# Optimization experiments

Hardware: AMD Instinct MI355X
Metric: run time of the kernel (lower is better)

Reference implementation:

```python
import jax, jax.numpy as jnp
import numpy as np

B, N, DIN, DOUT, H = 4, 2048, 512, 512, 8
HD = DOUT // H


def setup_inputs() -> dict:
    key = jax.random.key(0)
    ks = jax.random.split(key, 8)
    x = jax.random.normal(ks[0], (B, N, DIN), dtype=jnp.float32)
    mask = jax.random.randint(ks[1], (B, 1, N, N), 0, 2, dtype=jnp.int32)
    s = 1.0 / np.sqrt(DIN)
    Wq = jax.random.uniform(ks[2], (DOUT, DIN), jnp.float32, -s, s)
    Wk = jax.random.uniform(ks[3], (DOUT, DIN), jnp.float32, -s, s)
    Wv = jax.random.uniform(ks[4], (DOUT, DIN), jnp.float32, -s, s)
    bq = jax.random.uniform(ks[5], (DOUT,), jnp.float32, -s, s)
    bk = jax.random.uniform(ks[6], (DOUT,), jnp.float32, -s, s)
    bv = jax.random.uniform(ks[7], (DOUT,), jnp.float32, -s, s)
    return {"x": x, "Wq": Wq, "bq": bq, "Wk": Wk, "bk": bk, "Wv": Wv, "bv": bv, "mask": mask}


def reference(x, Wq, bq, Wk, bk, Wv, bv, mask):
    b, n, _ = x.shape
    # torch Linear: y = x @ W.T + b ; split heads -> [b, h, n, hd]
    def proj(W, bias):
        y = jnp.einsum('bnd,od->bno', x, W) + bias
        return y.reshape(b, n, H, HD).transpose(0, 2, 1, 3)
    Q, K, V = proj(Wq, bq), proj(Wk, bk), proj(Wv, bv)
    scores = jnp.einsum('bhnd,bhmd->bhnm', Q, K) / np.sqrt(HD).astype(np.float32)
    scores = jnp.where(mask == 0, jnp.float32(-1e9), scores)
    attn = jax.nn.softmax(scores, axis=-1)
    ctx = jnp.einsum('bhnm,bhmd->bhnd', attn, V)
    ctx = ctx.transpose(0, 2, 1, 3).reshape(b, n, DOUT)
    return jax.nn.elu(ctx)
```

## Files before the change

### kernel.cpp

```cpp
#include <hip/hip_runtime.h>
#include <math.h>
#include <stdint.h>

#define CB 4
#define CN 2048
#define CDIN 512
#define CDOUT 512
#define CH 8
#define CHD 64
#define CM (CB * CN)
#define CBH (CB * CH)
#define NKT (CN / 64)

typedef _Float16 f16x8 __attribute__((ext_vector_type(8)));
typedef _Float16 f16x4 __attribute__((ext_vector_type(4)));
typedef float    f32x4 __attribute__((ext_vector_type(4)));

#define QSCALE 0.1803368801111204f

#define PB_X  2048
#define PB_WQ 2176
#define PB_WK 2304
#define PB_WV 2432
#define PB_MB 3456

__global__ __launch_bounds__(256) void prep_kernel(
    const float* __restrict__ x,  _Float16* __restrict__ xh,
    const float* __restrict__ Wq, _Float16* __restrict__ wqh,
    const float* __restrict__ Wk, _Float16* __restrict__ wkh,
    const float* __restrict__ Wv, _Float16* __restrict__ wvh,
    const int* __restrict__ mask, unsigned long long* __restrict__ mbits)
{
    const int bx = blockIdx.x;
    if (bx >= PB_WV) {
        const int lane = threadIdx.x & 63;
        const int wv   = threadIdx.x >> 6;
        const int wbase = (bx - PB_WV) * 256 + wv * 64;
        unsigned long long myword = 0;
        #pragma unroll 8
        for (int it = 0; it < 64; ++it) {
            int v = mask[(size_t)(wbase + it) * 64 + lane];
            unsigned long long bal = __ballot(v != 0);
            if (lane == it) myword = bal;
        }
        mbits[wbase + lane] = myword;
        return;
    }
    const float* s; _Float16* d; int i;
    if (bx < PB_X)       { s = x;  d = xh;  i = bx * 2048 + threadIdx.x * 8; }
    else if (bx < PB_WQ) { s = Wq; d = wqh; i = (bx - PB_X)  * 2048 + threadIdx.x * 8; }
    else if (bx < PB_WK) { s = Wk; d = wkh; i = (bx - PB_WQ) * 2048 + threadIdx.x * 8; }
    else                 { s = Wv; d = wvh; i = (bx - PB_WK) * 2048 + threadIdx.x * 8; }
    float4 a = *(const float4*)&s[i];
    float4 b = *(const float4*)&s[i + 4];
    f16x8 h = {(_Float16)a.x, (_Float16)a.y, (_Float16)a.z, (_Float16)a.w,
               (_Float16)b.x, (_Float16)b.y, (_Float16)b.z, (_Float16)b.w};
    *(f16x8*)&d[i] = h;
}

__global__ __launch_bounds__(256) void proj_kernel(
    const _Float16* __restrict__ xh,
    const _Float16* __restrict__ Wqh, const float* __restrict__ bq,
    const _Float16* __restrict__ Wkh, const float* __restrict__ bk,
    const _Float16* __restrict__ Wvh, const float* __restrict__ bv,
    _Float16* __restrict__ Qf, _Float16* __restrict__ Kf, _Float16* __restrict__ Vt)
{
    const int z = blockIdx.z;
    const _Float16* W; const float* bias;
    if (z == 0)      { W = Wqh; bias = bq; }
    else if (z == 1) { W = Wkh; bias = bk; }
    else             { W = Wvh; bias = bv; }

    __shared__ _Float16 SM[2 * 128 * 72];

    const int tid  = threadIdx.x;
    const int m0   = blockIdx.x * 128;
    const int o0   = blockIdx.y * 128;
    const int lane = tid & 63, w = tid >> 6;
    const int il   = lane & 15, quad = lane >> 4;
    const int srow = tid >> 3, kc = (tid & 7) * 8;

    f32x4 acc[2][8] = {};
    f16x8 xr[4], wr[4];

    #pragma unroll
    for (int i = 0; i < 4; ++i) {
        xr[i] = *(const f16x8*)&xh[(size_t)(m0 + srow + i * 32) * CDIN + kc];
        wr[i] = *(const f16x8*)&W[(size_t)(o0 + srow + i * 32) * CDIN + kc];
    }

    for (int k0 = 0; k0 < CDIN; k0 += 64) {
        #pragma unroll
        for (int i = 0; i < 4; ++i) {
            *(f16x8*)&SM[(srow + i * 32) * 72 + kc] = xr[i];
            *(f16x8*)&SM[9216 + (srow + i * 32) * 72 + kc] = wr[i];
        }
        __syncthreads();

        if (k0 + 64 < CDIN) {
            #pragma unroll
            for (int i = 0; i < 4; ++i) {
                xr[i] = *(const f16x8*)&xh[(size_t)(m0 + srow + i * 32) * CDIN + k0 + 64 + kc];
                wr[i] = *(const f16x8*)&W[(size_t)(o0 + srow + i * 32) * CDIN + k0 + 64 + kc];
            }
        }

        #pragma unroll
        for (int dh = 0; dh < 2; ++dh) {
            f16x8 X0 = *(const f16x8*)&SM[(w * 32 + il) * 72 + dh * 32 + quad * 8];
            f16x8 X1 = *(const f16x8*)&SM[(w * 32 + 16 + il) * 72 + dh * 32 + quad * 8];
            if (z < 2) {
                #pragma unroll
                for (int s = 0; s < 8; ++s) {
                    f16x8 Wv_ = *(const f16x8*)&SM[9216 + (s * 16 + il) * 72 + dh * 32 + quad * 8];
                    acc[0][s] = __builtin_amdgcn_mfma_f32_16x16x32_f16(Wv_, X0, acc[0][s], 0, 0, 0);
                    acc[1][s] = __builtin_amdgcn_mfma_f32_16x16x32_f16(Wv_, X1, acc[1][s], 0, 0, 0);
                }
            } else {
                #pragma unroll
                for (int s = 0; s < 8; ++s) {
                    f16x8 Wv_ = *(const f16x8*)&SM[9216 + (s * 16 + il) * 72 + dh * 32 + quad * 8];
                    acc[0][s] = __builtin_amdgcn_mfma_f32_16x16x32_f16(X0, Wv_, acc[0][s], 0, 0, 0);
                    acc[1][s] = __builtin_amdgcn_mfma_f32_16x16x32_f16(X1, Wv_, acc[1][s], 0, 0, 0);
                }
            }
        }
        __syncthreads();
    }

    const int b  = m0 / CN;
    const int nb = m0 & (CN - 1);
    if (z < 2) {
        const float sc = (z == 0) ? QSCALE : 1.0f;
        #pragma unroll
        for (int s = 0; s < 8; ++s) {
            #pragma unroll
            for (int mi = 0; mi < 2; ++mi) {
                f16x4 pv;
                #pragma unroll
                for (int r = 0; r < 4; ++r)
                    pv[r] = (_Float16)((acc[mi][s][r] + bias[o0 + s * 16 + quad * 4 + r]) * sc);
                *(f16x4*)&SM[(w * 32 + mi * 16 + il) * 140 + s * 16 + quad * 4] = pv;
            }
        }
    } else {
        #pragma unroll
        for (int s = 0; s < 8; ++s) {
            const float bval = bias[o0 + s * 16 + il];
            #pragma unroll
            for (int mi = 0; mi < 2; ++mi) {
                f16x4 pv = {(_Float16)(acc[mi][s][0] + bval),
                            (_Float16)(acc[mi][s][1] + bval),
                            (_Float16)(acc[mi][s][2] + bval),
                            (_Float16)(acc[mi][s][3] + bval)};
                *(f16x4*)&SM[(s * 16 + il) * 140 + w * 32 + mi * 16 + quad * 4] = pv;
            }
        }
    }
    __syncthreads();

    const int uu   = tid & 127;
    const int hseg = tid >> 7;
    const int bh   = b * CH + (o0 >> 6) + hseg;
    if (z < 2) {
        _Float16* dst = ((z == 0) ? Qf : Kf) + ((size_t)bh * CN + nb) * CHD;
        #pragma unroll
        for (int k = 0; k < 8; ++k) {
            int n = k * 16 + (uu >> 3);
            int d = (uu & 7) * 8;
            *(f16x8*)&dst[(size_t)n * CHD + d] =
                *(const f16x8*)&SM[n * 140 + hseg * 64 + d];
        }
    } else {
        _Float16* dst = Vt + (size_t)bh * CHD * CN + nb;
        #pragma unroll
        for (int k = 0; k < 8; ++k) {
            int d = k * 8 + (uu >> 4);
            int n = (uu & 15) * 8;
            *(f16x8*)&dst[(size_t)d * CN + n] =
                *(const f16x8*)&SM[(hseg * 64 + d) * 140 + n];
        }
    }
}

__global__ __launch_bounds__(512, 4) void attn_kernel(
    const _Float16* __restrict__ Qf, const _Float16* __restrict__ Kf,
    const _Float16* __restrict__ Vt, const unsigned long long* __restrict__ mbits,
    float* __restrict__ out)
{
    __shared__ uint4 Ks4[2][64][8];
    __shared__ uint4 Vs4[2][64][8];
    __shared__ uint4 Ps4[8][32][8];

    const int tid  = threadIdx.x;
    const int q0   = blockIdx.x * 128;
    const int bh   = blockIdx.y;
    const int b    = bh >> 3, h = bh & 7;
    const int lane = tid & 63, w = tid >> 6;
    const int kg   = w >> 2;
    const int wi   = w & 3;
    const int il   = lane & 15, quad = lane >> 4;
    const int i7   = il & 7;

    const int gtid = tid & 255;
    const int srow = gtid >> 2;
    const int sg   = (gtid & 3) * 2;
    const int sw0  = sg       ^ (srow & 7);
    const int sw1  = (sg + 1) ^ (srow & 7);

    const int kb = kg * 1024;

    _Float16* Pw = (_Float16*)&Ps4[w][0][0];

    const _Float16* Qb = Qf + (size_t)bh * CN * CHD;
    const _Float16* Kb = Kf + (size_t)bh * CN * CHD;
    const _Float16* Vb = Vt + (size_t)bh * CHD * CN;

    const int qg0 = q0 + wi * 32 + il;
    const int qg1 = qg0 + 16;
    const unsigned long long* mrow0 = mbits + ((size_t)b * CN + qg0) * NKT + kg * 16;
    const unsigned long long* mrow1 = mbits + ((size_t)b * CN + qg1) * NKT + kg * 16;

    f16x8 Qa[2][2];
    Qa[0][0] = *(const f16x8*)&Qb[(size_t)qg0 * CHD + quad * 8];
    Qa[0][1] = *(const f16x8*)&Qb[(size_t)qg0 * CHD + 32 + quad * 8];
    Qa[1][0] = *(const f16x8*)&Qb[(size_t)qg1 * CHD + quad * 8];
    Qa[1][1] = *(const f16x8*)&Qb[(size_t)qg1 * CHD + 32 + quad * 8];

    const f16x8 ones = {1.f16, 1.f16, 1.f16, 1.f16, 1.f16, 1.f16, 1.f16, 1.f16};

    f32x4 oacc[2][4] = {};
    f32x4 lacc[2] = {};

    uint4 kA0, kA1, vA0, vA1;
    unsigned long long mn0, mn1;
    kA0 = *(const uint4*)&Kb[(size_t)(kb + srow) * CHD + sg * 8];
    kA1 = *(const uint4*)&Kb[(size_t)(kb + srow) * CHD + sg * 8 + 8];
    vA0 = *(const uint4*)&Vb[(size_t)srow * CN + kb + sg * 8];
    vA1 = *(const uint4*)&Vb[(size_t)srow * CN + kb + sg * 8 + 8];
    mn0 = mrow0[0];
    mn1 = mrow1[0];
    Ks4[kg][srow][sw0] = kA0; Ks4[kg][srow][sw1] = kA1;
    Vs4[kg][srow][sw0] = vA0; Vs4[kg][srow][sw1] = vA1;
    __syncthreads();

    for (int t = 0; t < 16; ++t) {
        const unsigned long long mc0 = mn0, mc1 = mn1;

        if (t < 15) {
            const size_t ko = (size_t)(kb + (t + 1) * 64 + srow) * CHD + sg * 8;
            kA0 = *(const uint4*)&Kb[ko];
            kA1 = *(const uint4*)&Kb[ko + 8];
            const size_t vo = (size_t)srow * CN + kb + (t + 1) * 64 + sg * 8;
            vA0 = *(const uint4*)&Vb[vo];
            vA1 = *(const uint4*)&Vb[vo + 8];
            mn0 = mrow0[t + 1];
            mn1 = mrow1[t + 1];
        }

        f32x4 st[2][4] = {};
        #pragma unroll
        for (int s = 0; s < 4; ++s) {
            f16x8 A0 = *(const f16x8*)&Ks4[kg][s * 16 + il][quad ^ i7];
            f16x8 A1 = *(const f16x8*)&Ks4[kg][s * 16 + il][(4 + quad) ^ i7];
            st[0][s] = __builtin_amdgcn_mfma_f32_16x16x32_f16(A0, Qa[0][0], st[0][s], 0, 0, 0);
            st[0][s] = __builtin_amdgcn_mfma_f32_16x16x32_f16(A1, Qa[0][1], st[0][s], 0, 0, 0);
            st[1][s] = __builtin_amdgcn_mfma_f32_16x16x32_f16(A0, Qa[1][0], st[1][s], 0, 0, 0);
            st[1][s] = __builtin_amdgcn_mfma_f32_16x16x32_f16(A1, Qa[1][1], st[1][s], 0, 0, 0);
        }

        #pragma unroll
        for (int g = 0; g < 2; ++g) {
            const unsigned long long mw = g ? mc1 : mc0;
            const uint32_t mlo = (uint32_t)mw, mhi = (uint32_t)(mw >> 32);
            #pragma unroll
            for (int s = 0; s < 4; ++s) {
                const uint32_t mm = (s < 2) ? mlo : mhi;
                const int base = ((s & 1) << 4) + quad * 4;
                f16x4 pv;
                #pragma unroll
                for (int r = 0; r < 4; ++r) {
                    float sv = ((mm >> (base + r)) & 1u) ? st[g][s][r] : -1e9f;
                    pv[r] = (_Float16)__builtin_amdgcn_exp2f(sv);
                }
                const int pg = (s * 2 + (quad >> 1)) ^ i7;
                *(f16x4*)&Pw[(g * 16 + il) * 64 + pg * 8 + (quad & 1) * 4] = pv;
            }
        }

        f16x8 Pa[2][2];
        #pragma unroll
        for (int g = 0; g < 2; ++g) {
            Pa[g][0] = *(const f16x8*)&Pw[(g * 16 + il) * 64 + (quad ^ i7) * 8];
            Pa[g][1] = *(const f16x8*)&Pw[(g * 16 + il) * 64 + ((4 + quad) ^ i7) * 8];
        }
        #pragma unroll
        for (int s = 0; s < 4; ++s) {
            f16x8 B0 = *(const f16x8*)&Vs4[kg][s * 16 + il][quad ^ i7];
            f16x8 B1 = *(const f16x8*)&Vs4[kg][s * 16 + il][(4 + quad) ^ i7];
            oacc[0][s] = __builtin_amdgcn_mfma_f32_16x16x32_f16(Pa[0][0], B0, oacc[0][s], 0, 0, 0);
            oacc[0][s] = __builtin_amdgcn_mfma_f32_16x16x32_f16(Pa[0][1], B1, oacc[0][s], 0, 0, 0);
            oacc[1][s] = __builtin_amdgcn_mfma_f32_16x16x32_f16(Pa[1][0], B0, oacc[1][s], 0, 0, 0);
            oacc[1][s] = __builtin_amdgcn_mfma_f32_16x16x32_f16(Pa[1][1], B1, oacc[1][s], 0, 0, 0);
        }
        lacc[0] = __builtin_amdgcn_mfma_f32_16x16x32_f16(Pa[0][0], ones, lacc[0], 0, 0, 0);
        lacc[0] = __builtin_amdgcn_mfma_f32_16x16x32_f16(Pa[0][1], ones, lacc[0], 0, 0, 0);
        lacc[1] = __builtin_amdgcn_mfma_f32_16x16x32_f16(Pa[1][0], ones, lacc[1], 0, 0, 0);
        lacc[1] = __builtin_amdgcn_mfma_f32_16x16x32_f16(Pa[1][1], ones, lacc[1], 0, 0, 0);

        if (t < 15) {
            __syncthreads();
            Ks4[kg][srow][sw0] = kA0; Ks4[kg][srow][sw1] = kA1;
            Vs4[kg][srow][sw0] = vA0; Vs4[kg][srow][sw1] = vA1;
            __syncthreads();
        }
    }

    __syncthreads();
    f32x4* Ob = (f32x4*)&Ps4[0][0][0];
    f32x4* Lb = (f32x4*)&Ks4[0][0][0];
    const int obase = (wi * 64 + lane) * 8;
    const int lbase = (wi * 64 + lane) * 2;
    if (kg == 1) {
        #pragma unroll
        for (int g = 0; g < 2; ++g)
            #pragma unroll
            for (int s = 0; s < 4; ++s)
                Ob[obase + ((g * 4 + s) ^ (lane & 7))] = oacc[g][s];
        Lb[lbase + (lane & 1)]       = lacc[0];
        Lb[lbase + ((lane & 1) ^ 1)] = lacc[1];
    }
    __syncthreads();
    if (kg == 0) {
        lacc[0] += Lb[lbase + (lane & 1)];
        lacc[1] += Lb[lbase + ((lane & 1) ^ 1)];
        #pragma unroll
        for (int g = 0; g < 2; ++g)
            #pragma unroll
            for (int s = 0; s < 4; ++s)
                oacc[g][s] += Ob[obase + ((g * 4 + s) ^ (lane & 7))];

        #pragma unroll
        for (int g = 0; g < 2; ++g) {
            #pragma unroll
            for (int s = 0; s < 4; ++s) {
                const int d = h * CHD + s * 16 + il;
                #pragma unroll
                for (int r = 0; r < 4; ++r) {
                    int n = q0 + wi * 32 + g * 16 + quad * 4 + r;
                    float c = oacc[g][s][r] / lacc[g][r];
                    out[((size_t)b * CN + n) * CDOUT + d] = c > 0.f ? c : expm1f(c);
                }
            }
        }
    }
}

extern "C" void kernel_launch(void* const* d_in, const int* in_sizes, int n_in,
                              void* d_out, int out_size, void* d_ws, size_t ws_size,
                              hipStream_t stream) {
    const float* x    = (const float*)d_in[0];
    const float* Wq   = (const float*)d_in[1];
    const float* bq   = (const float*)d_in[2];
    const float* Wk   = (const float*)d_in[3];
    const float* bk   = (const float*)d_in[4];
    const float* Wv   = (const float*)d_in[5];
    const float* bv   = (const float*)d_in[6];
    const int*   mask = (const int*)d_in[7];
    float* out = (float*)d_out;

    const size_t nx = (size_t)CM * CDIN;
    const size_t nw = (size_t)CDOUT * CDIN;
    const size_t nt = (size_t)CBH * CN * CHD;
    _Float16* xh  = (_Float16*)d_ws;
    _Float16* wqh = xh + nx;
    _Float16* wkh = wqh + nw;
    _Float16* wvh = wkh + nw;
    _Float16* Qf  = wvh + nw;
    _Float16* Kf  = Qf + nt;
    _Float16* Vt  = Kf + nt;
    unsigned long long* mbits = (unsigned long long*)(Vt + nt);

    prep_kernel<<<dim3(PB_MB), 256, 0, stream>>>(
        x, xh, Wq, wqh, Wk, wkh, Wv, wvh, mask, mbits);
    proj_kernel<<<dim3(CM / 128, CDOUT / 128, 3), 256, 0, stream>>>(
        xh, wqh, bq, wkh, bk, wvh, bv, Qf, Kf, Vt);
    attn_kernel<<<dim3(CN / 128, CBH), 512, 0, stream>>>(
        Qf, Kf, Vt, mbits, out);
}
```

Baseline: 216.0 us.

## Use direct global-to-LDS loads in projection, swizzle attention grid, add MFMA priorities

Rewrites the projection GEMM to load tiles straight from global memory into XOR-swizzled, double-buffered LDS with global_load_lds, replacing the register-staged copy and one barrier per k-step. It also splits the prep kernel into separate convert and mask-packing launches and runs the projection as three launches, one per matrix. In attention it remaps blocks so consecutive blocks spread across heads and query tiles, and raises wave priority around the MFMA sections. The extra launches add overhead, and the block remap changes L2 locality.

Result: slower. 333.5 us (+54.4%).

```diff
diff --git a/kernel.cpp b/kernel.cpp
--- a/kernel.cpp
+++ b/kernel.cpp
@@ -18,34 +18,24 @@
 
 #define QSCALE 0.1803368801111204f
 
+__device__ __forceinline__ void gl_lds16(const _Float16* g, _Float16* l) {
+    __builtin_amdgcn_global_load_lds(
+        (const __attribute__((address_space(1))) void*)g,
+        (__attribute__((address_space(3))) void*)l, 16, 0, 0);
+}
+
 #define PB_X  2048
 #define PB_WQ 2176
 #define PB_WK 2304
 #define PB_WV 2432
-#define PB_MB 3456
-
-__global__ __launch_bounds__(256) void prep_kernel(
+
+__global__ __launch_bounds__(256) void prep_cvt_kernel(
     const float* __restrict__ x,  _Float16* __restrict__ xh,
     const float* __restrict__ Wq, _Float16* __restrict__ wqh,
     const float* __restrict__ Wk, _Float16* __restrict__ wkh,
-    const float* __restrict__ Wv, _Float16* __restrict__ wvh,
-    const int* __restrict__ mask, unsigned long long* __restrict__ mbits)
+    const float* __restrict__ Wv, _Float16* __restrict__ wvh)
 {
     const int bx = blockIdx.x;
-    if (bx >= PB_WV) {
-        const int lane = threadIdx.x & 63;
-        const int wv   = threadIdx.x >> 6;
-        const int wbase = (bx - PB_WV) * 256 + wv * 64;
-        unsigned long long myword = 0;
-        #pragma unroll 8
-        for (int it = 0; it < 64; ++it) {
-            int v = mask[(size_t)(wbase + it) * 64 + lane];
-            unsigned long long bal = __ballot(v != 0);
-            if (lane == it) myword = bal;
-        }
-        mbits[wbase + lane] = myword;
-        return;
-    }
     const float* s; _Float16* d; int i;
     if (bx < PB_X)       { s = x;  d = xh;  i = bx * 2048 + threadIdx.x * 8; }
     else if (bx < PB_WQ) { s = Wq; d = wqh; i = (bx - PB_X)  * 2048 + threadIdx.x * 8; }
@@ -58,68 +48,85 @@
     *(f16x8*)&d[i] = h;
 }
 
+__global__ __launch_bounds__(256) void prep_mask_kernel(
+    const int* __restrict__ mask, unsigned long long* __restrict__ mbits)
+{
+    const int lane = threadIdx.x & 63;
+    const int wv   = threadIdx.x >> 6;
+    const int wbase = blockIdx.x * 256 + wv * 64;
+    unsigned long long myword = 0;
+    #pragma unroll 8
+    for (int it = 0; it < 64; ++it) {
+        int v = mask[(size_t)(wbase + it) * 64 + lane];
+        unsigned long long bal = __ballot(v != 0);
+        if (lane == it) myword = bal;
+    }
+    mbits[wbase + lane] = myword;
+}
+
 __global__ __launch_bounds__(256) void proj_kernel(
     const _Float16* __restrict__ xh,
     const _Float16* __restrict__ Wqh, const float* __restrict__ bq,
     const _Float16* __restrict__ Wkh, const float* __restrict__ bk,
     const _Float16* __restrict__ Wvh, const float* __restrict__ bv,
-    _Float16* __restrict__ Qf, _Float16* __restrict__ Kf, _Float16* __restrict__ Vt)
+    _Float16* __restrict__ Qf, _Float16* __restrict__ Kf, _Float16* __restrict__ Vt,
+    const int z)
 {
-    const int z = blockIdx.z;
     const _Float16* W; const float* bias;
     if (z == 0)      { W = Wqh; bias = bq; }
     else if (z == 1) { W = Wkh; bias = bk; }
     else             { W = Wvh; bias = bv; }
 
-    __shared__ _Float16 SM[2 * 128 * 72];
+    __shared__ _Float16 SH[2][2][128][64];
 
     const int tid  = threadIdx.x;
     const int m0   = blockIdx.x * 128;
     const int o0   = blockIdx.y * 128;
     const int lane = tid & 63, w = tid >> 6;
     const int il   = lane & 15, quad = lane >> 4;
-    const int srow = tid >> 3, kc = (tid & 7) * 8;
+    const int i7   = il & 7;
+
+    const int srow8 = lane >> 3;
+    const int srcg  = ((lane & 7) ^ srow8) * 8;
 
     f32x4 acc[2][8] = {};
-    f16x8 xr[4], wr[4];
 
     #pragma unroll
     for (int i = 0; i < 4; ++i) {
-        xr[i] = *(const f16x8*)&xh[(size_t)(m0 + srow + i * 32) * CDIN + kc];
-        wr[i] = *(const f16x8*)&W[(size_t)(o0 + srow + i * 32) * CDIN + kc];
-    }
-
-    for (int k0 = 0; k0 < CDIN; k0 += 64) {
-        #pragma unroll
-        for (int i = 0; i < 4; ++i) {
-            *(f16x8*)&SM[(srow + i * 32) * 72 + kc] = xr[i];
-            *(f16x8*)&SM[9216 + (srow + i * 32) * 72 + kc] = wr[i];
-        }
-        __syncthreads();
-
+        const int r0 = i * 32 + w * 8;
+        gl_lds16(&xh[(size_t)(m0 + r0 + srow8) * CDIN + srcg], &SH[0][0][r0][0]);
+        gl_lds16(&W [(size_t)(o0 + r0 + srow8) * CDIN + srcg], &SH[1][0][r0][0]);
+    }
+    __syncthreads();
+
+    int kb = 0;
+    for (int k0 = 0; k0 < CDIN; k0 += 64, kb ^= 1) {
         if (k0 + 64 < CDIN) {
             #pragma unroll
             for (int i = 0; i < 4; ++i) {
-                xr[i] = *(const f16x8*)&xh[(size_t)(m0 + srow + i * 32) * CDIN + k0 + 64 + kc];
-                wr[i] = *(const f16x8*)&W[(size_t)(o0 + srow + i * 32) * CDIN + k0 + 64 + kc];
+                const int r0 = i * 32 + w * 8;
+                gl_lds16(&xh[(size_t)(m0 + r0 + srow8) * CDIN + k0 + 64 + srcg],
+                         &SH[0][kb ^ 1][r0][0]);
+                gl_lds16(&W [(size_t)(o0 + r0 + srow8) * CDIN + k0 + 64 + srcg],
+                         &SH[1][kb ^ 1][r0][0]);
             }
         }
 
         #pragma unroll
         for (int dh = 0; dh < 2; ++dh) {
-            f16x8 X0 = *(const f16x8*)&SM[(w * 32 + il) * 72 + dh * 32 + quad * 8];
-            f16x8 X1 = *(const f16x8*)&SM[(w * 32 + 16 + il) * 72 + dh * 32 + quad * 8];
+            f16x8 X0 = *(const f16x8*)&SH[0][kb][w * 32 + il][((dh * 4 + quad) ^ i7) * 8];
+            f16x8 X1 = *(const f16x8*)&SH[0][kb][w * 32 + 16 + il][((dh * 4 + quad) ^ i7) * 8];
             if (z < 2) {
                 #pragma unroll
                 for (int s = 0; s < 8; ++s) {
-                    f16x8 Wv_ = *(const f16x8*)&SM[9216 + (s * 16 + il) * 72 + dh * 32 + quad * 8];
+                    f16x8 Wv_ = *(const f16x8*)&SH[1][kb][s * 16 + il][((dh * 4 + quad) ^ i7) * 8];
                     acc[0][s] = __builtin_amdgcn_mfma_f32_16x16x32_f16(Wv_, X0, acc[0][s], 0, 0, 0);
                     acc[1][s] = __builtin_amdgcn_mfma_f32_16x16x32_f16(Wv_, X1, acc[1][s], 0, 0, 0);
                 }
             } else {
                 #pragma unroll
                 for (int s = 0; s < 8; ++s) {
-                    f16x8 Wv_ = *(const f16x8*)&SM[9216 + (s * 16 + il) * 72 + dh * 32 + quad * 8];
+                    f16x8 Wv_ = *(const f16x8*)&SH[1][kb][s * 16 + il][((dh * 4 + quad) ^ i7) * 8];
                     acc[0][s] = __builtin_amdgcn_mfma_f32_16x16x32_f16(X0, Wv_, acc[0][s], 0, 0, 0);
                     acc[1][s] = __builtin_amdgcn_mfma_f32_16x16x32_f16(X1, Wv_, acc[1][s], 0, 0, 0);
                 }
@@ -128,6 +135,7 @@
         __syncthreads();
     }
 
+    _Float16* SM = (_Float16*)SH;
     const int b  = m0 / CN;
     const int nb = m0 & (CN - 1);
     if (z < 2) {
@@ -193,8 +201,10 @@
     __shared__ uint4 Ps4[8][32][8];
 
     const int tid  = threadIdx.x;
-    const int q0   = blockIdx.x * 128;
-    const int bh   = blockIdx.y;
+    const int lin  = blockIdx.x + gridDim.x * blockIdx.y;
+    const int swz  = (lin & 7) * 64 + (lin >> 3);
+    const int q0   = (swz & 15) * 128;
+    const int bh   = swz >> 4;
     const int b    = bh >> 3, h = bh & 7;
     const int lane = tid & 63, w = tid >> 6;
     const int kg   = w >> 2;
@@ -259,6 +269,7 @@
         }
 
         f32x4 st[2][4] = {};
+        __builtin_amdgcn_s_setprio(1);
         #pragma unroll
         for (int s = 0; s < 4; ++s) {
             f16x8 A0 = *(const f16x8*)&Ks4[kg][s * 16 + il][quad ^ i7];
@@ -268,6 +279,7 @@
             st[1][s] = __builtin_amdgcn_mfma_f32_16x16x32_f16(A0, Qa[1][0], st[1][s], 0, 0, 0);
             st[1][s] = __builtin_amdgcn_mfma_f32_16x16x32_f16(A1, Qa[1][1], st[1][s], 0, 0, 0);
         }
+        __builtin_amdgcn_s_setprio(0);
 
         #pragma unroll
         for (int g = 0; g < 2; ++g) {
@@ -294,6 +306,7 @@
             Pa[g][0] = *(const f16x8*)&Pw[(g * 16 + il) * 64 + (quad ^ i7) * 8];
             Pa[g][1] = *(const f16x8*)&Pw[(g * 16 + il) * 64 + ((4 + quad) ^ i7) * 8];
         }
+        __builtin_amdgcn_s_setprio(1);
         #pragma unroll
         for (int s = 0; s < 4; ++s) {
             f16x8 B0 = *(const f16x8*)&Vs4[kg][s * 16 + il][quad ^ i7];
@@ -307,6 +320,7 @@
         lacc[0] = __builtin_amdgcn_mfma_f32_16x16x32_f16(Pa[0][1], ones, lacc[0], 0, 0, 0);
         lacc[1] = __builtin_amdgcn_mfma_f32_16x16x32_f16(Pa[1][0], ones, lacc[1], 0, 0, 0);
         lacc[1] = __builtin_amdgcn_mfma_f32_16x16x32_f16(Pa[1][1], ones, lacc[1], 0, 0, 0);
+        __builtin_amdgcn_s_setprio(0);
 
         if (t < 15) {
             __syncthreads();
@@ -381,10 +395,12 @@
     _Float16* Vt  = Kf + nt;
     unsigned long long* mbits = (unsigned long long*)(Vt + nt);
 
-    prep_kernel<<<dim3(PB_MB), 256, 0, stream>>>(
-        x, xh, Wq, wqh, Wk, wkh, Wv, wvh, mask, mbits);
-    proj_kernel<<<dim3(CM / 128, CDOUT / 128, 3), 256, 0, stream>>>(
-        xh, wqh, bq, wkh, bk, wvh, bv, Qf, Kf, Vt);
+    prep_cvt_kernel<<<dim3(PB_WV), 256, 0, stream>>>(
+        x, xh, Wq, wqh, Wk, wkh, Wv, wvh);
+    prep_mask_kernel<<<dim3(1024), 256, 0, stream>>>(mask, mbits);
+    for (int z = 0; z < 3; ++z)
+        proj_kernel<<<dim3(CM / 128, CDOUT / 128), 256, 0, stream>>>(
+            xh, wqh, bq, wkh, bk, wvh, bv, Qf, Kf, Vt, z);
     attn_kernel<<<dim3(CN / 128, CBH), 512, 0, stream>>>(
         Qf, Kf, Vt, mbits, out);
 }
```
